# Performance work log

Measured on AMD Instinct MI355X. Metric: run time of the kernel, lower is better.

Reference implementation:

```python
import jax, jax.numpy as jnp
import numpy as np

BN_EPS = 1e-5

def _bn_relu(x, gamma, beta):
    # BatchNorm1d in training mode: batch stats over (B, N) per channel
    mean = jnp.mean(x, axis=(0, 1), keepdims=True)
    var = jnp.var(x, axis=(0, 1), keepdims=True)
    return jax.nn.relu((x - mean) * jax.lax.rsqrt(var + BN_EPS) * gamma + beta)

def setup_inputs() -> dict:
    key = jax.random.key(0)
    ks = jax.random.split(key, 8)
    B, N, S, C1, C2 = 8, 8192, 2048, 128, 256
    return {
        'xyz1': jax.random.normal(ks[0], (B, N, 3), jnp.float32),
        'xyz2': jax.random.normal(ks[1], (B, S, 3), jnp.float32),
        'points1': jax.random.normal(ks[2], (B, N, C1), jnp.float32),
        'points2': jax.random.normal(ks[3], (B, S, C2), jnp.float32),
        'w0': jax.random.normal(ks[4], (256, C1 + C2), jnp.float32) * 0.02,
        'b0': jnp.zeros((256,), jnp.float32),
        'g0': jnp.ones((256,), jnp.float32),
        'be0': jnp.zeros((256,), jnp.float32),
        'w1': jax.random.normal(ks[5], (128, 256), jnp.float32) * 0.02,
        'b1': jnp.zeros((128,), jnp.float32),
        'g1': jnp.ones((128,), jnp.float32),
        'be1': jnp.zeros((128,), jnp.float32),
    }

def reference(xyz1, xyz2, points1, points2, w0, b0, g0, be0, w1, b1, g1, be1):
    # squared pairwise distances [B, N, S]
    sq = (jnp.sum(xyz1 * xyz1, -1)[:, :, None]
          - 2.0 * jnp.einsum('bnc,bmc->bnm', xyz1, xyz2)
          + jnp.sum(xyz2 * xyz2, -1)[:, None, :])
    neg_d, idx = jax.lax.top_k(-sq, 3)          # smallest 3 distances
    dist = -neg_d                               # [B, N, 3]
    recip = 1.0 / (dist + 1e-8)
    weight = recip / jnp.sum(recip, -1, keepdims=True)
    gathered = jax.vmap(lambda p, i: p[i])(points2, idx)   # [B, N, 3, C2]
    interp = jnp.sum(gathered * weight[..., None], axis=2)  # [B, N, C2]
    x = jnp.concatenate([points1, interp], axis=-1)         # [B, N, C1+C2]
    x = _bn_relu(jnp.einsum('bnc,oc->bno', x, w0) + b0, g0, be0)
    x = _bn_relu(jnp.einsum('bnc,oc->bno', x, w1) + b1, g1, be1)
    return x
```

## Files before the change

kernel.cpp:

```cpp
#include <hip/hip_runtime.h>

#define B_  8
#define N_  8192
#define S_  2048
#define C1_ 128
#define C2_ 256
#define KA_ 384
#define H0_ 256
#define H1_ 128
#define R_  (B_ * N_)

typedef __bf16 bf16;
typedef __attribute__((ext_vector_type(2))) __bf16 bf16x2;
typedef __attribute__((ext_vector_type(4))) __bf16 bf16x4;
typedef __attribute__((ext_vector_type(8))) __bf16 bf16x8;
typedef __attribute__((ext_vector_type(4))) float f32x4;

__device__ __forceinline__ void gload_lds16(const void* g, void* l) {
    __builtin_amdgcn_global_load_lds(
        (const __attribute__((address_space(1))) void*)g,
        (__attribute__((address_space(3))) void*)l, 16, 0, 0);
}

__global__ __launch_bounds__(256) void prep_kernel(const float* __restrict__ w0,
                                                   const float* __restrict__ w1,
                                                   const float* __restrict__ xyz2,
                                                   bf16* __restrict__ Wbf0,
                                                   bf16* __restrict__ Wbf1,
                                                   float* __restrict__ stats,
                                                   float4* __restrict__ c4g)
{
    int blk = blockIdx.x, tid = threadIdx.x;
    if (blk < 96) {
        int i = blk * 256 + tid;
        float4 v = *(const float4*)(w0 + (size_t)i * 4);
        bf16x4 o = { (bf16)v.x, (bf16)v.y, (bf16)v.z, (bf16)v.w };
        *(bf16x4*)(Wbf0 + (size_t)i * 4) = o;
    } else if (blk < 128) {
        int i = (blk - 96) * 256 + tid;
        float4 v = *(const float4*)(w1 + (size_t)i * 4);
        bf16x4 o = { (bf16)v.x, (bf16)v.y, (bf16)v.z, (bf16)v.w };
        *(bf16x4*)(Wbf1 + (size_t)i * 4) = o;
    } else if (blk == 128) {
        #pragma unroll
        for (int k = 0; k < 3; ++k) stats[k * 256 + tid] = 0.f;
    } else {
        int i = (blk - 129) * 256 + tid;
        float x = xyz2[(size_t)i * 3 + 0];
        float y = xyz2[(size_t)i * 3 + 1];
        float z = xyz2[(size_t)i * 3 + 2];
        float4 c; c.x = x; c.y = y; c.z = z; c.w = x * x + y * y + z * z;
        c4g[i] = c;
    }
}

__global__ __launch_bounds__(256) void top3_interp_kernel(
    const float* __restrict__ xyz1, const float4* __restrict__ c4g,
    const float* __restrict__ points1, const float* __restrict__ points2,
    bf16* __restrict__ Abf)
{
    __shared__ float4 sc[S_];
    __shared__ float  md[64][4][3];
    __shared__ int    mi[64][4][3];
    __shared__ int    sidx[64][3];
    __shared__ float  sw[64][3];

    int swz = (blockIdx.x & 7) * 128 + (blockIdx.x >> 3);
    int b = swz >> 7;
    int ntile = swz & 127;

    const float4* cand = c4g + (size_t)b * S_;
    for (int i = threadIdx.x; i < S_; i += 256)
        sc[i] = cand[i];
    __syncthreads();

    const int q  = threadIdx.x >> 2;
    const int sp = threadIdx.x & 3;
    const size_t row = (size_t)b * N_ + ntile * 64 + q;
    const float ax = -2.f * xyz1[row * 3 + 0];
    const float ay = -2.f * xyz1[row * 3 + 1];
    const float az = -2.f * xyz1[row * 3 + 2];

    float m0 = 1e30f, m1 = 1e30f, m2 = 1e30f;
    int   j0 = 0, j1 = 0, j2 = 0;

    #pragma unroll 4
    for (int i = 0; i < S_ / 4; ++i) {
        int s = i * 4 + sp;
        float4 c = sc[s];
        float m = fmaf(ax, c.x, fmaf(ay, c.y, fmaf(az, c.z, c.w)));
        if (m < m2) {
            if (m < m1) {
                m2 = m1; j2 = j1;
                if (m < m0) { m1 = m0; j1 = j0; m0 = m; j0 = s; }
                else        { m1 = m;  j1 = s; }
            } else { m2 = m; j2 = s; }
        }
    }
    md[q][sp][0] = m0; md[q][sp][1] = m1; md[q][sp][2] = m2;
    mi[q][sp][0] = j0; mi[q][sp][1] = j1; mi[q][sp][2] = j2;
    __syncthreads();

    if (threadIdx.x < 64) {
        int qq = threadIdx.x;
        float d0 = md[qq][0][0], d1 = md[qq][0][1], d2 = md[qq][0][2];
        int   i0 = mi[qq][0][0], i1 = mi[qq][0][1], i2 = mi[qq][0][2];
        #pragma unroll
        for (int p = 1; p < 4; ++p) {
            #pragma unroll
            for (int j = 0; j < 3; ++j) {
                float d = md[qq][p][j]; int s = mi[qq][p][j];
                bool lt2 = (d < d2) || (d == d2 && s < i2);
                if (lt2) {
                    bool lt1 = (d < d1) || (d == d1 && s < i1);
                    if (lt1) {
                        d2 = d1; i2 = i1;
                        bool lt0 = (d < d0) || (d == d0 && s < i0);
                        if (lt0) { d1 = d0; i1 = i0; d0 = d; i0 = s; }
                        else     { d1 = d;  i1 = s; }
                    } else { d2 = d; i2 = s; }
                }
            }
        }
        size_t orow = (size_t)b * N_ + ntile * 64 + qq;
        float px = xyz1[orow * 3 + 0], py = xyz1[orow * 3 + 1], pz = xyz1[orow * 3 + 2];
        float pp = px * px + py * py + pz * pz;
        float r0 = 1.f / (d0 + pp + 1e-8f);
        float r1 = 1.f / (d1 + pp + 1e-8f);
        float r2 = 1.f / (d2 + pp + 1e-8f);
        float inv = 1.f / (r0 + r1 + r2);
        sidx[qq][0] = i0; sidx[qq][1] = i1; sidx[qq][2] = i2;
        sw[qq][0] = r0 * inv; sw[qq][1] = r1 * inv; sw[qq][2] = r2 * inv;
    }
    __syncthreads();

    const int wv = threadIdx.x >> 6, ln = threadIdx.x & 63;
    const size_t rowbase = (size_t)b * N_ + ntile * 64;
    const float* p2 = points2 + (size_t)b * S_ * C2_;
    for (int r = wv; r < 64; r += 4) {
        size_t orow = rowbase + r;
        int ia = sidx[r][0], ib = sidx[r][1], ic = sidx[r][2];
        float wa = sw[r][0], wb = sw[r][1], wc = sw[r][2];
        float4 va = *(const float4*)(p2 + (size_t)ia * C2_ + ln * 4);
        float4 vb = *(const float4*)(p2 + (size_t)ib * C2_ + ln * 4);
        float4 vc = *(const float4*)(p2 + (size_t)ic * C2_ + ln * 4);
        bf16x4 o = { (bf16)(wa * va.x + wb * vb.x + wc * vc.x),
                     (bf16)(wa * va.y + wb * vb.y + wc * vc.y),
                     (bf16)(wa * va.z + wb * vb.z + wc * vc.z),
                     (bf16)(wa * va.w + wb * vb.w + wc * vc.w) };
        *(bf16x4*)(Abf + orow * KA_ + C1_ + ln * 4) = o;

        float2 p = *(const float2*)(points1 + orow * C1_ + ln * 2);
        bf16x2 po = { (bf16)p.x, (bf16)p.y };
        *(bf16x2*)(Abf + orow * KA_ + ln * 2) = po;
    }
}

template<int K, int OT, bool OUTBF>
__global__ __launch_bounds__(256) void mfma_gemm_kernel(
    const bf16* __restrict__ A, const bf16* __restrict__ Wt, void* __restrict__ Cout,
    float* __restrict__ sums, float* __restrict__ sumsq)
{
    __shared__ bf16 As[128 * 32];
    __shared__ bf16 Bs[128 * 32];
    __shared__ float csum[128], csumsq[128];
    const int tid = threadIdx.x;
    const int lane = tid & 63, wave = tid >> 6;
    const int wr = wave >> 1, wc = wave & 1;
    const int r0 = blockIdx.x * 128, o0 = blockIdx.y * 128;

    f32x4 acc[4][4] = {};

    const int l15 = lane & 15, g = lane >> 4;
    const int slot = g ^ ((l15 >> 1) & 3);
    int a_off[4], b_off[4];
    #pragma unroll
    for (int m = 0; m < 4; ++m) a_off[m] = (wr * 64 + m * 16 + l15) * 32 + slot * 8;
    #pragma unroll
    for (int n = 0; n < 4; ++n) b_off[n] = (wc * 64 + n * 16 + l15) * 32 + slot * 8;

    const int c0 = tid, c1 = tid + 256;
    const int ar0 = c0 >> 2, ar1 = c1 >> 2;
    const int kb0 = ((c0 & 3) ^ ((ar0 >> 1) & 3)) * 8;
    const int kb1 = ((c1 & 3) ^ ((ar1 >> 1) & 3)) * 8;

    if (tid < 128) { csum[tid] = 0.f; csumsq[tid] = 0.f; }

    for (int k0 = 0; k0 < K; k0 += 32) {
        __syncthreads();
        gload_lds16(A  + (size_t)(r0 + ar0) * K + k0 + kb0, &As[c0 * 8]);
        gload_lds16(A  + (size_t)(r0 + ar1) * K + k0 + kb1, &As[c1 * 8]);
        gload_lds16(Wt + (size_t)(o0 + ar0) * K + k0 + kb0, &Bs[c0 * 8]);
        gload_lds16(Wt + (size_t)(o0 + ar1) * K + k0 + kb1, &Bs[c1 * 8]);
        __syncthreads();
        bf16x8 af[4], bfr[4];
        #pragma unroll
        for (int m = 0; m < 4; ++m) af[m]  = *(const bf16x8*)&As[a_off[m]];
        #pragma unroll
        for (int n = 0; n < 4; ++n) bfr[n] = *(const bf16x8*)&Bs[b_off[n]];
        #pragma unroll
        for (int m = 0; m < 4; ++m)
            #pragma unroll
            for (int n = 0; n < 4; ++n)
                acc[m][n] = __builtin_amdgcn_mfma_f32_16x16x32_bf16(af[m], bfr[n], acc[m][n], 0, 0, 0);
    }

    const int crow = r0 + wr * 64 + g * 4;
    const int ccol = o0 + wc * 64 + l15;
    #pragma unroll
    for (int m = 0; m < 4; ++m)
        #pragma unroll
        for (int n = 0; n < 4; ++n)
            #pragma unroll
            for (int j = 0; j < 4; ++j) {
                size_t off = (size_t)(crow + m * 16 + j) * OT + ccol + n * 16;
                if (OUTBF) ((bf16*)Cout)[off] = (bf16)acc[m][n][j];
                else       ((float*)Cout)[off] = acc[m][n][j];
            }

    #pragma unroll
    for (int n = 0; n < 4; ++n) {
        float s = 0.f, q = 0.f;
        #pragma unroll
        for (int m = 0; m < 4; ++m)
            #pragma unroll
            for (int j = 0; j < 4; ++j) {
                float v = acc[m][n][j];
                s += v; q = fmaf(v, v, q);
            }
        int col = wc * 64 + n * 16 + l15;
        atomicAdd(&csum[col], s);
        atomicAdd(&csumsq[col], q);
    }
    __syncthreads();
    if (tid < 128) {
        atomicAdd(&sums[o0 + tid], csum[tid]);
        atomicAdd(&sumsq[o0 + tid], csumsq[tid]);
    }
}

__global__ __launch_bounds__(256) void mfma_gemm2_kernel(
    const bf16* __restrict__ Ahp, const bf16* __restrict__ Wt,
    const float* __restrict__ sums0, const float* __restrict__ sumsq0,
    const float* __restrict__ g0, const float* __restrict__ be0,
    float* __restrict__ Cout, float* __restrict__ sums, float* __restrict__ sumsq)
{
    constexpr int K = H0_, OT = H1_;
    __shared__ bf16 As[128 * 32];
    __shared__ bf16 Bs[128 * 32];
    __shared__ float csum[128], csumsq[128];
    __shared__ float sscale[256], sshift[256];
    const int tid = threadIdx.x;
    const int lane = tid & 63, wave = tid >> 6;
    const int wr = wave >> 1, wc = wave & 1;
    const int r0 = blockIdx.x * 128, o0 = blockIdx.y * 128;

    {
        const float invR = 1.f / (float)R_;
        float mean = sums0[tid] * invR;
        float var = sumsq0[tid] * invR - mean * mean;
        float sv = g0[tid] * rsqrtf(var + 1e-5f);
        sscale[tid] = sv;
        sshift[tid] = be0[tid] - mean * sv;
    }
    if (tid < 128) { csum[tid] = 0.f; csumsq[tid] = 0.f; }
    __syncthreads();

    f32x4 acc[4][4] = {};

    const int l15 = lane & 15, g = lane >> 4;
    const int slot = g ^ ((l15 >> 1) & 3);
    int a_off[4], b_off[4];
    #pragma unroll
    for (int m = 0; m < 4; ++m) a_off[m] = (wr * 64 + m * 16 + l15) * 32 + slot * 8;
    #pragma unroll
    for (int n = 0; n < 4; ++n) b_off[n] = (wc * 64 + n * 16 + l15) * 32 + slot * 8;

    const int c0 = tid, c1 = tid + 256;
    const int ar0 = c0 >> 2, ar1 = c1 >> 2;
    const int kb0 = ((c0 & 3) ^ ((ar0 >> 1) & 3)) * 8;
    const int kb1 = ((c1 & 3) ^ ((ar1 >> 1) & 3)) * 8;

    for (int k0 = 0; k0 < K; k0 += 32) {
        bf16x8 va0 = *(const bf16x8*)(Ahp + (size_t)(r0 + ar0) * K + k0 + kb0);
        bf16x8 va1 = *(const bf16x8*)(Ahp + (size_t)(r0 + ar1) * K + k0 + kb1);
        float s0a[8], h0a[8], s1a[8], h1a[8];
        *(float4*)&s0a[0] = *(const float4*)(&sscale[k0 + kb0]);
        *(float4*)&s0a[4] = *(const float4*)(&sscale[k0 + kb0 + 4]);
        *(float4*)&h0a[0] = *(const float4*)(&sshift[k0 + kb0]);
        *(float4*)&h0a[4] = *(const float4*)(&sshift[k0 + kb0 + 4]);
        *(float4*)&s1a[0] = *(const float4*)(&sscale[k0 + kb1]);
        *(float4*)&s1a[4] = *(const float4*)(&sscale[k0 + kb1 + 4]);
        *(float4*)&h1a[0] = *(const float4*)(&sshift[k0 + kb1]);
        *(float4*)&h1a[4] = *(const float4*)(&sshift[k0 + kb1 + 4]);
        bf16x8 ra0, ra1;
        #pragma unroll
        for (int j = 0; j < 8; ++j) {
            float f0 = fmaxf(0.f, fmaf((float)va0[j], s0a[j], h0a[j]));
            float f1 = fmaxf(0.f, fmaf((float)va1[j], s1a[j], h1a[j]));
            ra0[j] = (bf16)f0; ra1[j] = (bf16)f1;
        }
        __syncthreads();
        gload_lds16(Wt + (size_t)(o0 + ar0) * K + k0 + kb0, &Bs[c0 * 8]);
        gload_lds16(Wt + (size_t)(o0 + ar1) * K + k0 + kb1, &Bs[c1 * 8]);
        *(bf16x8*)&As[c0 * 8] = ra0;
        *(bf16x8*)&As[c1 * 8] = ra1;
        __syncthreads();
        bf16x8 af[4], bfr[4];
        #pragma unroll
        for (int m = 0; m < 4; ++m) af[m]  = *(const bf16x8*)&As[a_off[m]];
        #pragma unroll
        for (int n = 0; n < 4; ++n) bfr[n] = *(const bf16x8*)&Bs[b_off[n]];
        #pragma unroll
        for (int m = 0; m < 4; ++m)
            #pragma unroll
            for (int n = 0; n < 4; ++n)
                acc[m][n] = __builtin_amdgcn_mfma_f32_16x16x32_bf16(af[m], bfr[n], acc[m][n], 0, 0, 0);
    }

    const int crow = r0 + wr * 64 + g * 4;
    const int ccol = o0 + wc * 64 + l15;
    #pragma unroll
    for (int m = 0; m < 4; ++m)
        #pragma unroll
        for (int n = 0; n < 4; ++n)
            #pragma unroll
            for (int j = 0; j < 4; ++j)
                ((float*)Cout)[(size_t)(crow + m * 16 + j) * OT + ccol + n * 16] = acc[m][n][j];

    #pragma unroll
    for (int n = 0; n < 4; ++n) {
        float s = 0.f, q = 0.f;
        #pragma unroll
        for (int m = 0; m < 4; ++m)
            #pragma unroll
            for (int j = 0; j < 4; ++j) {
                float v = acc[m][n][j];
                s += v; q = fmaf(v, v, q);
            }
        int col = wc * 64 + n * 16 + l15;
        atomicAdd(&csum[col], s);
        atomicAdd(&csumsq[col], q);
    }
    __syncthreads();
    if (tid < 128) {
        atomicAdd(&sums[o0 + tid], csum[tid]);
        atomicAdd(&sumsq[o0 + tid], csumsq[tid]);
    }
}

__global__ __launch_bounds__(256) void bnrelu_kernel(
    float* __restrict__ X, const float* __restrict__ sums1,
    const float* __restrict__ sumsq1, const float* __restrict__ g1,
    const float* __restrict__ be1)
{
    __shared__ float ss[128], sh[128];
    int tid = threadIdx.x;
    if (tid < 128) {
        const float invR = 1.f / (float)R_;
        float mean = sums1[tid] * invR;
        float var = sumsq1[tid] * invR - mean * mean;
        float sv = g1[tid] * rsqrtf(var + 1e-5f);
        ss[tid] = sv;
        sh[tid] = be1[tid] - mean * sv;
    }
    __syncthreads();

    #pragma unroll
    for (int it = 0; it < 4; ++it) {
        size_t i = (size_t)it * 524288 + (size_t)blockIdx.x * 256 + tid;
        int c = ((int)i & 31) * 4;
        float4 v = *(float4*)(X + i * 4);
        v.x = fmaxf(0.f, v.x * ss[c + 0] + sh[c + 0]);
        v.y = fmaxf(0.f, v.y * ss[c + 1] + sh[c + 1]);
        v.z = fmaxf(0.f, v.z * ss[c + 2] + sh[c + 2]);
        v.w = fmaxf(0.f, v.w * ss[c + 3] + sh[c + 3]);
        *(float4*)(X + i * 4) = v;
    }
}

extern "C" void kernel_launch(void* const* d_in, const int* in_sizes, int n_in,
                              void* d_out, int out_size, void* d_ws, size_t ws_size,
                              hipStream_t stream)
{
    const float* xyz1    = (const float*)d_in[0];
    const float* xyz2    = (const float*)d_in[1];
    const float* points1 = (const float*)d_in[2];
    const float* points2 = (const float*)d_in[3];
    const float* w0  = (const float*)d_in[4];
    const float* g0  = (const float*)d_in[6];
    const float* be0 = (const float*)d_in[7];
    const float* w1  = (const float*)d_in[8];
    const float* g1  = (const float*)d_in[10];
    const float* be1 = (const float*)d_in[11];
    float* out = (float*)d_out;
    char* ws = (char*)d_ws;

    bf16* Abf     = (bf16*)(ws);
    bf16* hpre_bf = (bf16*)(ws + 50331648);
    bf16* Wbf0    = (bf16*)(ws + 117440512);
    bf16* Wbf1    = (bf16*)(ws + 117637120);
    float* stats  = (float*)(ws + 119275520);
    float4* c4g   = (float4*)(ws + 119279616);
    float* sums0 = stats,        *sumsq0 = stats + 256;
    float* sums1 = stats + 512,  *sumsq1 = stats + 640;

    prep_kernel<<<193, 256, 0, stream>>>(w0, w1, xyz2, Wbf0, Wbf1, stats, c4g);
    top3_interp_kernel<<<B_ * (N_ / 64), 256, 0, stream>>>(xyz1, c4g, points1, points2, Abf);

    mfma_gemm_kernel<KA_, H0_, true><<<dim3(R_ / 128, 2), 256, 0, stream>>>(
        Abf, Wbf0, hpre_bf, sums0, sumsq0);

    mfma_gemm2_kernel<<<dim3(R_ / 128, 1), 256, 0, stream>>>(
        hpre_bf, Wbf1, sums0, sumsq0, g0, be0, out, sums1, sumsq1);

    bnrelu_kernel<<<2048, 256, 0, stream>>>(out, sums1, sumsq1, g1, be1);
}
```

Baseline: 159.2 us.

## Fuse final BN+ReLU into second GEMM via cooperative grid sync

The second GEMM now runs as a cooperative kernel with one block per 128-row tile. After the per-channel statistics are accumulated atomically, a grid-wide sync lets every block compute the BN scale and shift and apply BN+ReLU to its register accumulators before a single store. This removes the separate bnrelu kernel and its full read-modify-write pass over the output. The cost is that all 512 blocks must be co-resident, hence the occupancy hint, and the grid barrier adds its own latency.

```diff
diff --git a/kernel.cpp b/kernel.cpp
--- a/kernel.cpp
+++ b/kernel.cpp
@@ -1,4 +1,7 @@
 #include <hip/hip_runtime.h>
+#include <hip/hip_cooperative_groups.h>
+
+namespace cg = cooperative_groups;
 
 #define B_  8
 #define N_  8192
@@ -239,10 +242,11 @@
     }
 }
 
-__global__ __launch_bounds__(256) void mfma_gemm2_kernel(
+__global__ __launch_bounds__(256, 2) void mfma_gemm2_kernel(
     const bf16* __restrict__ Ahp, const bf16* __restrict__ Wt,
     const float* __restrict__ sums0, const float* __restrict__ sumsq0,
     const float* __restrict__ g0, const float* __restrict__ be0,
+    const float* __restrict__ g1, const float* __restrict__ be1,
     float* __restrict__ Cout, float* __restrict__ sums, float* __restrict__ sumsq)
 {
     constexpr int K = H0_, OT = H1_;
@@ -253,7 +257,7 @@
     const int tid = threadIdx.x;
     const int lane = tid & 63, wave = tid >> 6;
     const int wr = wave >> 1, wc = wave & 1;
-    const int r0 = blockIdx.x * 128, o0 = blockIdx.y * 128;
+    const int r0 = blockIdx.x * 128, o0 = 0;
 
     {
         const float invR = 1.f / (float)R_;
@@ -318,16 +322,6 @@
                 acc[m][n] = __builtin_amdgcn_mfma_f32_16x16x32_bf16(af[m], bfr[n], acc[m][n], 0, 0, 0);
     }
 
-    const int crow = r0 + wr * 64 + g * 4;
-    const int ccol = o0 + wc * 64 + l15;
-    #pragma unroll
-    for (int m = 0; m < 4; ++m)
-        #pragma unroll
-        for (int n = 0; n < 4; ++n)
-            #pragma unroll
-            for (int j = 0; j < 4; ++j)
-                ((float*)Cout)[(size_t)(crow + m * 16 + j) * OT + ccol + n * 16] = acc[m][n][j];
-
     #pragma unroll
     for (int n = 0; n < 4; ++n) {
         float s = 0.f, q = 0.f;
@@ -344,38 +338,37 @@
     }
     __syncthreads();
     if (tid < 128) {
-        atomicAdd(&sums[o0 + tid], csum[tid]);
-        atomicAdd(&sumsq[o0 + tid], csumsq[tid]);
-    }
-}
-
-__global__ __launch_bounds__(256) void bnrelu_kernel(
-    float* __restrict__ X, const float* __restrict__ sums1,
-    const float* __restrict__ sumsq1, const float* __restrict__ g1,
-    const float* __restrict__ be1)
-{
-    __shared__ float ss[128], sh[128];
-    int tid = threadIdx.x;
+        atomicAdd(&sums[tid], csum[tid]);
+        atomicAdd(&sumsq[tid], csumsq[tid]);
+    }
+    __threadfence();
+    cg::this_grid().sync();
+
     if (tid < 128) {
         const float invR = 1.f / (float)R_;
-        float mean = sums1[tid] * invR;
-        float var = sumsq1[tid] * invR - mean * mean;
+        float sv_sum = __hip_atomic_load(&sums[tid], __ATOMIC_RELAXED, __HIP_MEMORY_SCOPE_AGENT);
+        float sv_sq  = __hip_atomic_load(&sumsq[tid], __ATOMIC_RELAXED, __HIP_MEMORY_SCOPE_AGENT);
+        float mean = sv_sum * invR;
+        float var = sv_sq * invR - mean * mean;
         float sv = g1[tid] * rsqrtf(var + 1e-5f);
-        ss[tid] = sv;
-        sh[tid] = be1[tid] - mean * sv;
-    }
-    __syncthreads();
-
-    #pragma unroll
-    for (int it = 0; it < 4; ++it) {
-        size_t i = (size_t)it * 524288 + (size_t)blockIdx.x * 256 + tid;
-        int c = ((int)i & 31) * 4;
-        float4 v = *(float4*)(X + i * 4);
-        v.x = fmaxf(0.f, v.x * ss[c + 0] + sh[c + 0]);
-        v.y = fmaxf(0.f, v.y * ss[c + 1] + sh[c + 1]);
-        v.z = fmaxf(0.f, v.z * ss[c + 2] + sh[c + 2]);
-        v.w = fmaxf(0.f, v.w * ss[c + 3] + sh[c + 3]);
-        *(float4*)(X + i * 4) = v;
+        csum[tid] = sv;
+        csumsq[tid] = be1[tid] - mean * sv;
+    }
+    __syncthreads();
+
+    const int crow = r0 + wr * 64 + g * 4;
+    const int ccol = o0 + wc * 64 + l15;
+    #pragma unroll
+    for (int n = 0; n < 4; ++n) {
+        int col = ccol + n * 16;
+        float sv = csum[col], sh = csumsq[col];
+        #pragma unroll
+        for (int m = 0; m < 4; ++m)
+            #pragma unroll
+            for (int j = 0; j < 4; ++j) {
+                float v = fmaxf(0.f, fmaf(acc[m][n][j], sv, sh));
+                Cout[(size_t)(crow + m * 16 + j) * OT + col] = v;
+            }
     }
 }
 
@@ -411,8 +404,9 @@
     mfma_gemm_kernel<KA_, H0_, true><<<dim3(R_ / 128, 2), 256, 0, stream>>>(
         Abf, Wbf0, hpre_bf, sums0, sumsq0);
 
-    mfma_gemm2_kernel<<<dim3(R_ / 128, 1), 256, 0, stream>>>(
-        hpre_bf, Wbf1, sums0, sumsq0, g0, be0, out, sums1, sumsq1);
-
-    bnrelu_kernel<<<2048, 256, 0, stream>>>(out, sums1, sumsq1, g1, be1);
-}
+    void* args[] = { (void*)&hpre_bf, (void*)&Wbf1, (void*)&sums0, (void*)&sumsq0,
+                     (void*)&g0, (void*)&be0, (void*)&g1, (void*)&be1,
+                     (void*)&out, (void*)&sums1, (void*)&sumsq1 };
+    hipLaunchCooperativeKernel((void*)mfma_gemm2_kernel, dim3(R_ / 128), dim3(256),
+                               args, 0, stream);
+}
```

Result: slower. 244.1 us (+53.3%).
